# Performance work log

Hardware: AMD Instinct MI355X
Metric: run time of the kernel (lower is better)

The kernel has to match this reference:

```python
import jax, jax.numpy as jnp
import numpy as np


def _conv1x1(x, w, b=None):
    # x: (N,C,H,W), w: (O,C) -> (N,O,H,W)
    y = jnp.einsum('nchw,oc->nohw', x, w)
    return y if b is None else y + b[None, :, None, None]


def _norm(f):
    # per-channel zero-mean / unit-std over (N,H,W); torch.std is unbiased (ddof=1)
    mean = f.mean(axis=(0, 2, 3), keepdims=True)
    std = f.std(axis=(0, 2, 3), ddof=1, keepdims=True)
    return (f - mean) / (std + 1e-6)


def _causal_attention(x, w_cls):
    N, C, H, W = x.shape
    M = _conv1x1(x, w_cls).reshape(N, -1, H * W)     # (N,K,HW)
    sm = jax.nn.softmax(M, axis=2)                   # softmax over spatial
    return jnp.einsum('nkp,ncp->nkc', sm, x.reshape(N, C, H * W))  # (N,K,C)


def _ccnet(x, wq, bq, wk, bk, wv, bv, gamma1):
    B, C, H, W = x.shape
    q = _conv1x1(x, wq, bq)  # (B,Cq,H,W)
    k = _conv1x1(x, wk, bk)
    v = _conv1x1(x, wv, bv)  # (B,C,H,W)
    # column (vertical) attention energies with -inf on the self diagonal
    eH = jnp.einsum('bciw,bcjw->biwj', q, k)         # (B,H,W,H)
    eH = jnp.where(jnp.eye(H, dtype=bool)[None, :, None, :], -jnp.inf, eH)
    # row (horizontal) attention energies
    eW = jnp.einsum('bchi,bchj->bhij', q, k)         # (B,H,W,W)
    att = jax.nn.softmax(jnp.concatenate([eH, eW], axis=3), axis=3)
    attH, attW = att[..., :H], att[..., H:]
    outH = jnp.einsum('bcjw,biwj->bciw', v, attH)    # aggregate along column
    outW = jnp.einsum('bchj,bhij->bchi', v, attW)    # aggregate along row
    return gamma1 * (outH + outW) + x


def setup_inputs() -> dict:
    key = jax.random.key(0)
    ks = jax.random.split(key, 10)
    B, C, H, W = 8, 256, 96, 96
    Cq, K = C // 8, 6
    f32 = jnp.float32
    return {
        'preds_S': jax.random.normal(ks[0], (B, C, H, W), f32),
        'preds_T': jax.random.normal(ks[1], (B, C, H, W), f32),
        'w_cls': jax.random.normal(ks[2], (K, C), f32) * 0.05,
        'wq': jax.random.normal(ks[3], (Cq, C), f32) * 0.05,
        'bq': jnp.zeros((Cq,), f32),
        'wk': jax.random.normal(ks[4], (Cq, C), f32) * 0.05,
        'bk': jnp.zeros((Cq,), f32),
        'wv': jax.random.normal(ks[5], (C, C), f32) * 0.05,
        'bv': jnp.zeros((C,), f32),
        'gamma1': jax.random.normal(ks[6], (1,), f32) * 0.1,
    }


def reference(preds_S, preds_T, w_cls, wq, bq, wk, bk, wv, bv, gamma1):
    CA_W, CC_W = 0.0005, 1e-05
    N = preds_S.shape[0]
    s = _norm(preds_S)
    t = _norm(preds_T)
    ca_t = _causal_attention(t, w_cls)
    ca_s = _causal_attention(s, w_cls)
    ca_loss = jnp.sum((ca_t - ca_s) ** 2) / N
    cc_t = _ccnet(t, wq, bq, wk, bk, wv, bv, gamma1)
    cc_s = _ccnet(s, wq, bq, wk, bk, wv, bv, gamma1)
    cc_loss = jnp.sum((cc_t - cc_s) ** 2) / N
    return ca_loss * CA_W + cc_loss * CC_W
```

## Files before the change

### kernel.cpp

```cpp
#include <hip/hip_runtime.h>
#include <math.h>

#define NBAT 8
#define NC   256
#define NH   96
#define NW   96
#define NP   9216
#define NCQ  32
#define NKC  6
#define NV   320
#define NTOT 73728

typedef __attribute__((ext_vector_type(4))) float  floatx4;
typedef __attribute__((ext_vector_type(8))) short  short8;

__device__ __forceinline__ float bf2f(unsigned short h){
  return __uint_as_float(((unsigned)h) << 16);
}
__device__ __forceinline__ unsigned short f2bf(float f){
  unsigned u = __float_as_uint(f);
  u += 0x7FFFu + ((u >> 16) & 1u);
  return (unsigned short)(u >> 16);
}

union F4 { float4 v; float a[4]; };

__device__ __forceinline__ float warpReduceSum(float v){
  #pragma unroll
  for (int m = 32; m; m >>= 1) v += __shfl_xor(v, m);
  return v;
}
__device__ __forceinline__ float warpReduceMax(float v){
  #pragma unroll
  for (int m = 32; m; m >>= 1) v = fmaxf(v, __shfl_xor(v, m));
  return v;
}
__device__ float blockReduceSum(float v){
  __shared__ float lds[8];
  v = warpReduceSum(v);
  int wid = threadIdx.x >> 6, lane = threadIdx.x & 63;
  int nw = blockDim.x >> 6;
  if (lane == 0) lds[wid] = v;
  __syncthreads();
  if (wid == 0){
    v = (lane < nw) ? lds[lane] : 0.f;
    #pragma unroll
    for (int m = 4; m; m >>= 1) v += __shfl_xor(v, m);
  }
  __syncthreads();
  return v;
}
__device__ float blockReduceMax(float v){
  __shared__ float lds[8];
  v = warpReduceMax(v);
  int wid = threadIdx.x >> 6, lane = threadIdx.x & 63;
  int nw = blockDim.x >> 6;
  if (lane == 0) lds[wid] = v;
  __syncthreads();
  if (wid == 0){
    v = (lane < nw) ? lds[lane] : -INFINITY;
    #pragma unroll
    for (int m = 4; m; m >>= 1) v = fmaxf(v, __shfl_xor(v, m));
  }
  __syncthreads();
  return v;
}

__global__ __launch_bounds__(256)
void k_stats(const float* __restrict__ S, const float* __restrict__ T,
             float* __restrict__ s_sum, float* __restrict__ s_sq){
  int blk = blockIdx.x;
  int t = blk / (NC * NBAT);
  int rem = blk % (NC * NBAT);
  int c = rem / NBAT;
  int n = rem % NBAT;
  const float4* x4 = (const float4*)((t ? T : S) + ((size_t)n * NC + c) * NP);
  F4 f[9];
  #pragma unroll
  for (int j = 0; j < 9; j++) f[j].v = x4[threadIdx.x + j * 256];
  float s = 0.f, q = 0.f;
  #pragma unroll
  for (int j = 0; j < 9; j++)
    #pragma unroll
    for (int e = 0; e < 4; e++){ s += f[j].a[e]; q += f[j].a[e] * f[j].a[e]; }
  s = blockReduceSum(s);
  q = blockReduceSum(q);
  if (threadIdx.x == 0){
    atomicAdd(&s_sum[t * NC + c], s);
    atomicAdd(&s_sq[t * NC + c], q);
  }
}

__global__ __launch_bounds__(512)
void k_finalize(const float* __restrict__ s_sum, const float* __restrict__ s_sq,
                float* __restrict__ mean, float* __restrict__ inv){
  int i = threadIdx.x;
  if (i < 2 * NC){
    float s = s_sum[i], q = s_sq[i];
    float m = s / (float)NTOT;
    float var = (q - s * m) / (float)(NTOT - 1);
    var = fmaxf(var, 0.f);
    mean[i] = m;
    inv[i] = 1.f / (sqrtf(var) + 1e-6f);
  }
}

__global__ __launch_bounds__(256)
void k_xn(const float* __restrict__ S, const float* __restrict__ T, int b0,
          const float* __restrict__ mean, const float* __restrict__ inv,
          unsigned short* __restrict__ XNT, unsigned short* __restrict__ XNS){
  int pt = blockIdx.x, ct = blockIdx.y;
  int bb = blockIdx.z >> 1, ts = blockIdx.z & 1;
  int t = ts ? 0 : 1;
  const float* x0 = ts ? S : T;
  unsigned short* XN = (ts ? XNS : XNT) + (size_t)bb * NP * NC;
  int bg = b0 + bb;
  int p0 = pt * 64, c0 = ct * 64;
  __shared__ float tile[64 * 65];
  const float* x = x0 + ((size_t)bg * NC + c0) * NP + p0;
  #pragma unroll
  for (int i = 0; i < 4; i++){
    int idx = threadIdx.x + i * 256;
    int r = idx >> 4, g = (idx & 15) * 4;
    F4 f; f.v = *(const float4*)(x + (size_t)r * NP + g);
    float m = mean[t * NC + c0 + r], iv = inv[t * NC + c0 + r];
    #pragma unroll
    for (int j = 0; j < 4; j++) tile[(g + j) * 65 + r] = (f.a[j] - m) * iv;
  }
  __syncthreads();
  #pragma unroll
  for (int i = 0; i < 4; i++){
    int idx = threadIdx.x + i * 256;
    int p = idx >> 4, g = (idx & 15) * 4;
    unsigned lo = (unsigned)f2bf(tile[p * 65 + g + 0]) | ((unsigned)f2bf(tile[p * 65 + g + 1]) << 16);
    unsigned hi = (unsigned)f2bf(tile[p * 65 + g + 2]) | ((unsigned)f2bf(tile[p * 65 + g + 3]) << 16);
    uint2 u; u.x = lo; u.y = hi;
    *(uint2*)(XN + ((size_t)(p0 + p)) * NC + c0 + g) = u;
  }
}

__global__ __launch_bounds__(256)
void k_caM(const unsigned short* __restrict__ XNT, const unsigned short* __restrict__ XNS,
           const float* __restrict__ wcls, int b0,
           float* __restrict__ smca){
  int pt = blockIdx.x, bb = blockIdx.y, ts = blockIdx.z;
  int t = ts ? 0 : 1;
  const unsigned short* XN = (ts ? XNS : XNT) + (size_t)bb * NP * NC;
  __shared__ float wcf[NKC * NC];
  for (int idx = threadIdx.x; idx < NKC * NC; idx += 256) wcf[idx] = wcls[idx];
  __syncthreads();
  int p = pt * 256 + threadIdx.x;
  const unsigned short* row = XN + (size_t)p * NC;
  float acc[NKC];
  #pragma unroll
  for (int k = 0; k < NKC; k++) acc[k] = 0.f;
  for (int c = 0; c < NC; c += 8){
    short8 v = *(const short8*)(row + c);
    #pragma unroll
    for (int j = 0; j < 8; j++){
      float xv = bf2f((unsigned short)v[j]);
      #pragma unroll
      for (int k = 0; k < NKC; k++) acc[k] += wcf[k * NC + c + j] * xv;
    }
  }
  size_t base = ((size_t)(t * NBAT + b0 + bb) * NKC) * NP + p;
  #pragma unroll
  for (int k = 0; k < NKC; k++) smca[base + (size_t)k * NP] = acc[k];
}

__global__ __launch_bounds__(256)
void k_caSoftmax(float* __restrict__ smca, int b0){
  int r = blockIdx.x;
  int bb = r / (2 * NKC);
  int rem = r % (2 * NKC);
  int ts = rem / NKC, k = rem % NKC;
  int t = ts ? 0 : 1;
  float* row = smca + ((size_t)(t * NBAT + b0 + bb) * NKC + k) * NP;
  float m = -INFINITY;
  for (int p = threadIdx.x; p < NP; p += 256) m = fmaxf(m, row[p]);
  m = blockReduceMax(m);
  __shared__ float bm, bs;
  if (threadIdx.x == 0) bm = m;
  __syncthreads();
  m = bm;
  float s = 0.f;
  for (int p = threadIdx.x; p < NP; p += 256) s += expf(row[p] - m);
  s = blockReduceSum(s);
  if (threadIdx.x == 0) bs = 1.f / s;
  __syncthreads();
  float rs = bs;
  for (int p = threadIdx.x; p < NP; p += 256) row[p] = expf(row[p] - m) * rs;
}

__global__ __launch_bounds__(256)
void k_caOut(const unsigned short* __restrict__ XNT, const unsigned short* __restrict__ XNS,
             const float* __restrict__ smca, int b0,
             float* __restrict__ ca){
  int ks = blockIdx.x, bb = blockIdx.y, ts = blockIdx.z;
  int t = ts ? 0 : 1;
  const unsigned short* XN = (ts ? XNS : XNT) + (size_t)bb * NP * NC;
  int p0 = ks * 256;
  __shared__ float smt[NKC * 256];
  const float* smbase = smca + (size_t)(t * NBAT + b0 + bb) * NKC * NP;
  for (int idx = threadIdx.x; idx < NKC * 256; idx += 256){
    int k = idx >> 8, pp = idx & 255;
    smt[idx] = smbase[(size_t)k * NP + p0 + pp];
  }
  __syncthreads();
  int c = threadIdx.x;
  float acc[NKC];
  #pragma unroll
  for (int k = 0; k < NKC; k++) acc[k] = 0.f;
  const unsigned short* xp = XN + (size_t)p0 * NC + c;
  for (int pp = 0; pp < 256; pp++){
    float xv = bf2f(xp[(size_t)pp * NC]);
    #pragma unroll
    for (int k = 0; k < NKC; k++) acc[k] += smt[k * 256 + pp] * xv;
  }
  float* cab = ca + ((size_t)(t * NBAT + b0 + bb) * NKC) * NC + c;
  #pragma unroll
  for (int k = 0; k < NKC; k++) atomicAdd(&cab[(size_t)k * NC], acc[k]);
}

__global__ __launch_bounds__(256)
void k_caLoss(const float* __restrict__ ca, float* __restrict__ out){
  int i = blockIdx.x * 256 + threadIdx.x;
  float d = 0.f;
  if (i < NBAT * NKC * NC) d = ca[(size_t)NBAT * NKC * NC + i] - ca[i];
  float ss = blockReduceSum(d * d);
  if (threadIdx.x == 0) atomicAdd(out, ss * (0.0005f / 8.0f));
}

__global__ __launch_bounds__(256)
void k_wconv(const float* __restrict__ wv, const float* __restrict__ wq,
             const float* __restrict__ wk, unsigned short* __restrict__ Wb){
  int n = blockIdx.x;
  const float* src = (n < 256) ? (wv + (size_t)n * NC)
                   : (n < 288) ? (wq + (size_t)(n - 256) * NC)
                               : (wk + (size_t)(n - 288) * NC);
  Wb[(size_t)n * NC + threadIdx.x] = f2bf(src[threadIdx.x]);
}

__global__ __launch_bounds__(256)
void k_v(const unsigned short* __restrict__ XNT, const unsigned short* __restrict__ XNS,
         const unsigned short* __restrict__ Wb,
         const float* __restrict__ bv, const float* __restrict__ bq,
         const float* __restrict__ bk,
         unsigned short* __restrict__ V1T, unsigned short* __restrict__ V1S,
         unsigned short* __restrict__ qT, unsigned short* __restrict__ kT,
         unsigned short* __restrict__ qS, unsigned short* __restrict__ kS){
  int pt = blockIdx.x;
  int bb = blockIdx.y >> 1, ts = blockIdx.y & 1;
  const unsigned short* XN = (ts ? XNS : XNT) + (size_t)bb * NP * NC;
  unsigned short* V1 = (ts ? V1S : V1T) + (size_t)bb * NP * NC;
  unsigned short* qb  = (ts ? qS : qT) + (size_t)bb * NP * NCQ;
  unsigned short* kb  = (ts ? kS : kT) + (size_t)bb * NP * NCQ;
  int p0 = pt * 64;
  __shared__ unsigned short Wl[NV * 40];
  int lane = threadIdx.x & 63;
  int wid = threadIdx.x >> 6;
  int col = lane & 15, quad = lane >> 4;
  const unsigned short* xnb = XN + (size_t)(p0 + wid * 16 + col) * NC;
  floatx4 acc[20];
  #pragma unroll
  for (int nt = 0; nt < 20; nt++) acc[nt] = (floatx4){0.f, 0.f, 0.f, 0.f};

  int ci_n[5], ci_k8[5];
  #pragma unroll
  for (int i = 0; i < 5; i++){ int ci = i * 256 + threadIdx.x; ci_n[i] = ci >> 2; ci_k8[i] = (ci & 3) * 8; }

  short8 w[5];
  #pragma unroll
  for (int i = 0; i < 5; i++)
    w[i] = *(const short8*)(Wb + (size_t)ci_n[i] * NC + ci_k8[i]);

  for (int ks = 0; ks < 8; ks++){
    if (ks) __syncthreads();
    #pragma unroll
    for (int i = 0; i < 5; i++)
      *(short8*)(Wl + ci_n[i] * 40 + ci_k8[i]) = w[i];
    __syncthreads();
    if (ks < 7){
      int k0n = (ks + 1) * 32;
      #pragma unroll
      for (int i = 0; i < 5; i++)
        w[i] = *(const short8*)(Wb + (size_t)ci_n[i] * NC + k0n + ci_k8[i]);
    }
    short8 a = *(const short8*)(xnb + ks * 32 + quad * 8);
    #pragma unroll
    for (int nt = 0; nt < 20; nt++){
      short8 b = *(const short8*)(Wl + (nt * 16 + col) * 40 + quad * 8);
      acc[nt] = __builtin_amdgcn_mfma_f32_16x16x32_bf16(a, b, acc[nt], 0, 0, 0);
    }
  }

  int prow0 = p0 + wid * 16 + quad * 4;
  int hh = prow0 / 96, ww = prow0 % 96;
  #pragma unroll
  for (int nt = 0; nt < 16; nt++){
    int c = nt * 16 + col;
    float bias = bv[c];
    uint2 u;
    u.x = (unsigned)f2bf(acc[nt][0] + bias) | ((unsigned)f2bf(acc[nt][1] + bias) << 16);
    u.y = (unsigned)f2bf(acc[nt][2] + bias) | ((unsigned)f2bf(acc[nt][3] + bias) << 16);
    *(uint2*)(V1 + ((size_t)(hh * 256 + c)) * 96 + ww) = u;
  }
  #pragma unroll
  for (int nt = 16; nt < 18; nt++){
    int c = (nt - 16) * 16 + col;
    float bias = bq[c];
    #pragma unroll
    for (int i = 0; i < 4; i++)
      qb[((size_t)(prow0 + i)) * NCQ + c] = f2bf(acc[nt][i] + bias);
  }
  #pragma unroll
  for (int nt = 18; nt < 20; nt++){
    int c = (nt - 18) * 16 + col;
    float bias = bk[c];
    #pragma unroll
    for (int i = 0; i < 4; i++)
      kb[((size_t)(prow0 + i)) * NCQ + c] = f2bf(acc[nt][i] + bias);
  }
}

__global__ __launch_bounds__(256)
void k_vt(const unsigned short* __restrict__ V1T, const unsigned short* __restrict__ V1S,
          unsigned short* __restrict__ V2T, unsigned short* __restrict__ V2S){
  int cp = blockIdx.x;
  int bb = blockIdx.y >> 1, ts = blockIdx.y & 1;
  const unsigned short* V1 = (ts ? V1S : V1T) + (size_t)bb * NP * NC;
  unsigned short* V2 = (ts ? V2S : V2T) + (size_t)bb * NP * NC;
  int c0 = cp * 2;
  __shared__ unsigned short tile[2 * 96 * 104];
  #pragma unroll
  for (int k = 0; k < 9; k++){
    int idx = threadIdx.x + k * 256;
    int cl = idx / 1152, rem = idx % 1152;
    int h = rem / 12, g = rem % 12;
    short8 v = *(const short8*)(V1 + ((size_t)(h * 256 + c0 + cl)) * 96 + g * 8);
    #pragma unroll
    for (int jj = 0; jj < 8; jj++)
      tile[cl * 9984 + (g * 8 + jj) * 104 + h] = ((unsigned short*)&v)[jj];
  }
  __syncthreads();
  #pragma unroll
  for (int k = 0; k < 9; k++){
    int idx = threadIdx.x + k * 256;
    int cl = idx / 1152, rem = idx % 1152;
    int w = rem / 12, g = rem % 12;
    short8 v = *(const short8*)(tile + cl * 9984 + w * 104 + g * 8);
    *(short8*)(V2 + ((size_t)(w * 256 + c0 + cl)) * 96 + g * 8) = v;
  }
}

__global__ __launch_bounds__(256)
void k_e(const unsigned short* __restrict__ qT, const unsigned short* __restrict__ kT,
         const unsigned short* __restrict__ qS, const unsigned short* __restrict__ kS,
         unsigned short* __restrict__ attHtT, unsigned short* __restrict__ attWT,
         unsigned short* __restrict__ attHtS, unsigned short* __restrict__ attWS){
  int x = blockIdx.x, which = blockIdx.z;
  int bb = blockIdx.y >> 1, ts = blockIdx.y & 1;
  const unsigned short* qb = (ts ? qS : qT) + (size_t)bb * NP * NCQ;
  const unsigned short* kb = (ts ? kS : kT) + (size_t)bb * NP * NCQ;
  unsigned short* att = (which ? (ts ? attWS : attWT) : (ts ? attHtS : attHtT))
                        + (size_t)bb * NP * 96;
  int lane = threadIdx.x & 63, wid = threadIdx.x >> 6;
  int col = lane & 15, quad = lane >> 4;
  int mi0 = (wid & 1) * 3, ni0 = (wid >> 1) * 3;
  short8 a[3], b[3];
  if (which == 0){
    #pragma unroll
    for (int m = 0; m < 3; m++)
      a[m] = *(const short8*)(qb + ((size_t)(((mi0 + m) * 16 + col) * 96 + x)) * NCQ + quad * 8);
    #pragma unroll
    for (int n = 0; n < 3; n++)
      b[n] = *(const short8*)(kb + ((size_t)(((ni0 + n) * 16 + col) * 96 + x)) * NCQ + quad * 8);
  } else {
    #pragma unroll
    for (int m = 0; m < 3; m++)
      a[m] = *(const short8*)(qb + ((size_t)(x * 96 + (mi0 + m) * 16 + col)) * NCQ + quad * 8);
    #pragma unroll
    for (int n = 0; n < 3; n++)
      b[n] = *(const short8*)(kb + ((size_t)(x * 96 + (ni0 + n) * 16 + col)) * NCQ + quad * 8);
  }
  floatx4 acc[3][3];
  #pragma unroll
  for (int m = 0; m < 3; m++)
    #pragma unroll
    for (int n = 0; n < 3; n++){
      acc[m][n] = (floatx4){0.f, 0.f, 0.f, 0.f};
      acc[m][n] = __builtin_amdgcn_mfma_f32_16x16x32_bf16(a[m], b[n], acc[m][n], 0, 0, 0);
    }
  #pragma unroll
  for (int m = 0; m < 3; m++)
    #pragma unroll
    for (int n = 0; n < 3; n++){
      int j = (ni0 + n) * 16 + col;
      #pragma unroll
      for (int r = 0; r < 4; r++){
        int i = (mi0 + m) * 16 + quad * 4 + r;
        float v = (!which && j == i) ? -INFINITY : acc[m][n][r];
        att[((size_t)(x * 96 + i)) * 96 + j] = f2bf(v);
      }
    }
}

__global__ __launch_bounds__(256)
void k_attSoftmax(unsigned short* __restrict__ attHtT, unsigned short* __restrict__ attWT,
                  unsigned short* __restrict__ attHtS, unsigned short* __restrict__ attWS,
                  int nbp){
  int q = blockIdx.x * 4 + (threadIdx.x >> 6);
  int lane = threadIdx.x & 63;
  int sS = (q >= nbp);
  int ql = sS ? q - nbp : q;
  unsigned short* aHt = sS ? attHtS : attHtT;
  unsigned short* aW  = sS ? attWS  : attWT;
  int bb = ql / NP, p = ql % NP;
  unsigned short* rowW = aW  + ((size_t)(bb * NP + p)) * 96;
  unsigned short* rowH = aHt + ((size_t)(bb * NP + (p % 96) * 96 + p / 96)) * 96;
  float h0 = bf2f(rowH[lane]);
  float w0 = bf2f(rowW[lane]);
  float h1 = (lane < 32) ? bf2f(rowH[64 + lane]) : -INFINITY;
  float w1 = (lane < 32) ? bf2f(rowW[64 + lane]) : -INFINITY;
  float m = fmaxf(fmaxf(h0, h1), fmaxf(w0, w1));
  m = warpReduceMax(m);
  float xh0 = expf(h0 - m), xw0 = expf(w0 - m);
  float xh1 = (lane < 32) ? expf(h1 - m) : 0.f;
  float xw1 = (lane < 32) ? expf(w1 - m) : 0.f;
  float s = warpReduceSum(xh0 + xw0 + xh1 + xw1);
  float rs = 1.f / s;
  rowH[lane] = f2bf(xh0 * rs);
  rowW[lane] = f2bf(xw0 * rs);
  if (lane < 32){
    rowH[64 + lane] = f2bf(xh1 * rs);
    rowW[64 + lane] = f2bf(xw1 * rs);
  }
}

__global__ __launch_bounds__(256)
void k_outH(const unsigned short* __restrict__ V2T, const unsigned short* __restrict__ V2S,
            const unsigned short* __restrict__ attHtT, const unsigned short* __restrict__ attHtS,
            unsigned short* __restrict__ OHT, unsigned short* __restrict__ OHS){
  int w = blockIdx.x, cs = blockIdx.z;
  int bb = blockIdx.y >> 1, ts = blockIdx.y & 1;
  const unsigned short* V2 = (ts ? V2S : V2T) + (size_t)bb * NP * NC;
  const unsigned short* att = (ts ? attHtS : attHtT) + (size_t)bb * NP * 96;
  unsigned short* OH = (ts ? OHS : OHT) + (size_t)bb * NP * NC + (size_t)cs * NP * 64;
  int lane = threadIdx.x & 63, wid = threadIdx.x >> 6;
  int col = lane & 15, quad = lane >> 4;
  int cl = wid * 16 + col;
  int c = cs * 64 + cl;
  floatx4 acc[6];
  #pragma unroll
  for (int m = 0; m < 6; m++) acc[m] = (floatx4){0.f, 0.f, 0.f, 0.f};
  #pragma unroll
  for (int ks = 0; ks < 3; ks++){
    int k0 = ks * 32 + quad * 8;
    short8 a[6], b;
    #pragma unroll
    for (int m = 0; m < 6; m++)
      a[m] = *(const short8*)(att + ((size_t)(w * 96 + m * 16 + col)) * 96 + k0);
    b = *(const short8*)(V2 + ((size_t)(w * 256 + c)) * 96 + k0);
    #pragma unroll
    for (int m = 0; m < 6; m++)
      acc[m] = __builtin_amdgcn_mfma_f32_16x16x32_bf16(a[m], b, acc[m], 0, 0, 0);
  }
  #pragma unroll
  for (int m = 0; m < 6; m++){
    #pragma unroll
    for (int r = 0; r < 4; r++){
      int i = m * 16 + quad * 4 + r;
      OH[((size_t)(i * 96 + w)) * 64 + cl] = f2bf(acc[m][r]);
    }
  }
}

__global__ __launch_bounds__(256)
void k_outWL(const unsigned short* __restrict__ V1T, const unsigned short* __restrict__ attWT,
             const unsigned short* __restrict__ OHT,
             const unsigned short* __restrict__ V1S, const unsigned short* __restrict__ attWS,
             const unsigned short* __restrict__ OHS,
             const unsigned short* __restrict__ XNT, const unsigned short* __restrict__ XNS,
             const float* __restrict__ gamma,
             float* __restrict__ out){
  int h = blockIdx.x, bb = blockIdx.y, cs = blockIdx.z;
  size_t pb = (size_t)bb * NP * NC;
  int lane = threadIdx.x & 63, wid = threadIdx.x >> 6;
  int col = lane & 15, quad = lane >> 4;
  int cl = wid * 16 + col;
  int c  = cs * 64 + cl;

  __shared__ unsigned short ohTl[96 * 72];
  __shared__ unsigned short ohSl[96 * 72];
  __shared__ unsigned short dnl [96 * 72];

  const unsigned short* OHTb = OHT + pb + (size_t)cs * NP * 64 + (size_t)(h * 96) * 64;
  const unsigned short* OHSb = OHS + pb + (size_t)cs * NP * 64 + (size_t)(h * 96) * 64;
  #pragma unroll
  for (int k = 0; k < 3; k++){
    int g = threadIdx.x + k * 256;
    int i = g >> 3, cc = (g & 7) * 8;
    short8 ot = *(const short8*)(OHTb + g * 8);
    short8 os = *(const short8*)(OHSb + g * 8);
    size_t gx = pb + ((size_t)(h * 96 + i)) * NC + cs * 64 + cc;
    short8 xt = *(const short8*)(XNT + gx);
    short8 xs = *(const short8*)(XNS + gx);
    short8 dn;
    #pragma unroll
    for (int j = 0; j < 8; j++)
      ((unsigned short*)&dn)[j] = f2bf(bf2f((unsigned short)xt[j]) - bf2f((unsigned short)xs[j]));
    *(short8*)(ohTl + i * 72 + cc) = ot;
    *(short8*)(ohSl + i * 72 + cc) = os;
    *(short8*)(dnl  + i * 72 + cc) = dn;
  }
  __syncthreads();

  floatx4 accT[6], accS[6];
  #pragma unroll
  for (int m = 0; m < 6; m++){
    accT[m] = (floatx4){0.f, 0.f, 0.f, 0.f};
    accS[m] = (floatx4){0.f, 0.f, 0.f, 0.f};
  }
  #pragma unroll
  for (int ks = 0; ks < 3; ks++){
    int k0 = ks * 32 + quad * 8;
    short8 a[6], b;
    #pragma unroll
    for (int m = 0; m < 6; m++)
      a[m] = *(const short8*)(attWT + (size_t)bb * NP * 96 + ((size_t)(h * 96 + m * 16 + col)) * 96 + k0);
    b = *(const short8*)(V1T + pb + ((size_t)(h * 256 + c)) * 96 + k0);
    #pragma unroll
    for (int m = 0; m < 6; m++)
      accT[m] = __builtin_amdgcn_mfma_f32_16x16x32_bf16(a[m], b, accT[m], 0, 0, 0);
  }
  #pragma unroll
  for (int ks = 0; ks < 3; ks++){
    int k0 = ks * 32 + quad * 8;
    short8 a[6], b;
    #pragma unroll
    for (int m = 0; m < 6; m++)
      a[m] = *(const short8*)(attWS + (size_t)bb * NP * 96 + ((size_t)(h * 96 + m * 16 + col)) * 96 + k0);
    b = *(const short8*)(V1S + pb + ((size_t)(h * 256 + c)) * 96 + k0);
    #pragma unroll
    for (int m = 0; m < 6; m++)
      accS[m] = __builtin_amdgcn_mfma_f32_16x16x32_bf16(a[m], b, accS[m], 0, 0, 0);
  }

  float g = gamma[0];
  float ss = 0.f;
  #pragma unroll
  for (int m = 0; m < 6; m++){
    int i0 = m * 16 + quad * 4;
    #pragma unroll
    for (int r = 0; r < 4; r++){
      int i = i0 + r;
      float oT = accT[m][r] + bf2f(ohTl[i * 72 + cl]);
      float oS = accS[m][r] + bf2f(ohSl[i * 72 + cl]);
      float d = g * (oT - oS) + bf2f(dnl[i * 72 + cl]);
      ss += d * d;
    }
  }
  ss = blockReduceSum(ss);
  if (threadIdx.x == 0) atomicAdd(out, ss * (1e-5f / 8.0f));
}

extern "C" void kernel_launch(void* const* d_in, const int* in_sizes, int n_in,
                              void* d_out, int out_size, void* d_ws, size_t ws_size,
                              hipStream_t stream){
  (void)in_sizes; (void)n_in; (void)out_size;
  const float* S    = (const float*)d_in[0];
  const float* T    = (const float*)d_in[1];
  const float* wcls = (const float*)d_in[2];
  const float* wq   = (const float*)d_in[3];
  const float* bq   = (const float*)d_in[4];
  const float* wk   = (const float*)d_in[5];
  const float* bk   = (const float*)d_in[6];
  const float* wv   = (const float*)d_in[7];
  const float* bv   = (const float*)d_in[8];
  const float* gamma= (const float*)d_in[9];
  float* out = (float*)d_out;

  char* base = (char*)d_ws;
  size_t off = 0;
  auto alloc = [&](size_t b){ size_t o = off; off += (b + 255) & ~(size_t)255; return o; };
  size_t o_ssum = alloc(2 * NC * 4);
  size_t o_ssq  = alloc(2 * NC * 4);
  size_t o_mean = alloc(2 * NC * 4);
  size_t o_inv  = alloc(2 * NC * 4);
  size_t o_wb   = alloc((size_t)NV * NC * 2);
  size_t o_ca   = alloc((size_t)2 * NBAT * NKC * NC * 4);
  size_t o_smca = alloc((size_t)2 * NBAT * NKC * NP * 4);
  size_t fixed = off;

  const size_t PB  = (size_t)NP * NC * 2;
  const size_t AT1 = (size_t)NP * 96 * 2;
  const size_t QB  = (size_t)NP * NCQ * 2;
  size_t per_b = 8 * PB + 4 * AT1 + 4 * QB;
  int NB = 8;
  while (NB > 1 && fixed + (size_t)NB * per_b + 8192 > ws_size) NB >>= 1;

  size_t o_xnT = alloc((size_t)NB * PB);
  size_t o_xnS = alloc((size_t)NB * PB);
  size_t o_v1T = alloc((size_t)NB * PB);
  size_t o_v1S = alloc((size_t)NB * PB);
  size_t o_v2T = alloc((size_t)NB * PB);
  size_t o_v2S = alloc((size_t)NB * PB);
  size_t o_ohT = alloc((size_t)NB * PB);
  size_t o_ohS = alloc((size_t)NB * PB);
  size_t o_hT  = alloc((size_t)NB * AT1);
  size_t o_wT  = alloc((size_t)NB * AT1);
  size_t o_hS  = alloc((size_t)NB * AT1);
  size_t o_wS  = alloc((size_t)NB * AT1);
  size_t o_qT  = alloc((size_t)NB * QB);
  size_t o_kT  = alloc((size_t)NB * QB);
  size_t o_qS  = alloc((size_t)NB * QB);
  size_t o_kS  = alloc((size_t)NB * QB);

  float* ssum = (float*)(base + o_ssum);
  float* ssq  = (float*)(base + o_ssq);
  float* mean = (float*)(base + o_mean);
  float* inv  = (float*)(base + o_inv);
  float* ca   = (float*)(base + o_ca);
  float* smca = (float*)(base + o_smca);
  unsigned short* Wb   = (unsigned short*)(base + o_wb);
  unsigned short* XNT  = (unsigned short*)(base + o_xnT);
  unsigned short* XNS  = (unsigned short*)(base + o_xnS);
  unsigned short* V1T  = (unsigned short*)(base + o_v1T);
  unsigned short* V1S  = (unsigned short*)(base + o_v1S);
  unsigned short* V2T  = (unsigned short*)(base + o_v2T);
  unsigned short* V2S  = (unsigned short*)(base + o_v2S);
  unsigned short* OHT  = (unsigned short*)(base + o_ohT);
  unsigned short* OHS  = (unsigned short*)(base + o_ohS);
  unsigned short* aHtT = (unsigned short*)(base + o_hT);
  unsigned short* aWT  = (unsigned short*)(base + o_wT);
  unsigned short* aHtS = (unsigned short*)(base + o_hS);
  unsigned short* aWS  = (unsigned short*)(base + o_wS);
  unsigned short* qT   = (unsigned short*)(base + o_qT);
  unsigned short* kT   = (unsigned short*)(base + o_kT);
  unsigned short* qS   = (unsigned short*)(base + o_qS);
  unsigned short* kS   = (unsigned short*)(base + o_kS);

  hipMemsetAsync(d_out, 0, 4, stream);
  hipMemsetAsync(base + o_ssum, 0, 4096, stream);
  hipMemsetAsync(base + o_ca, 0, (size_t)2 * NBAT * NKC * NC * 4, stream);

  k_stats<<<dim3(2 * NC * NBAT), 256, 0, stream>>>(S, T, ssum, ssq);
  k_finalize<<<1, 512, 0, stream>>>(ssum, ssq, mean, inv);
  k_wconv<<<dim3(NV), 256, 0, stream>>>(wv, wq, wk, Wb);

  for (int b0 = 0; b0 < NBAT; b0 += NB){
    k_xn<<<dim3(144, 4, 2 * NB), 256, 0, stream>>>(S, T, b0, mean, inv, XNT, XNS);
    k_caM<<<dim3(36, NB, 2), 256, 0, stream>>>(XNT, XNS, wcls, b0, smca);
    k_caSoftmax<<<dim3(2 * NB * NKC), 256, 0, stream>>>(smca, b0);
    k_caOut<<<dim3(36, NB, 2), 256, 0, stream>>>(XNT, XNS, smca, b0, ca);
    k_v<<<dim3(144, 2 * NB), 256, 0, stream>>>(XNT, XNS, Wb, bv, bq, bk,
                                               V1T, V1S, qT, kT, qS, kS);
    k_vt<<<dim3(128, 2 * NB), 256, 0, stream>>>(V1T, V1S, V2T, V2S);
    k_e<<<dim3(96, 2 * NB, 2), 256, 0, stream>>>(qT, kT, qS, kS, aHtT, aWT, aHtS, aWS);
    k_attSoftmax<<<dim3(2 * NB * NP / 4), 256, 0, stream>>>(aHtT, aWT, aHtS, aWS, NB * NP);
    k_outH<<<dim3(96, 2 * NB, 4), 256, 0, stream>>>(V2T, V2S, aHtT, aHtS, OHT, OHS);
    k_outWL<<<dim3(96, NB, 4), 256, 0, stream>>>(V1T, aWT, OHT, V1S, aWS, OHS,
                                                 XNT, XNS, gamma, out);
  }
  k_caLoss<<<dim3(48), 256, 0, stream>>>(ca, out);
}
```

Before: 611.1 us.

## Fuse CA logits into normalize kernel, precompute T-S diff, alias V2 buffers

The normalization kernel now handles teacher and student in one block. It also writes a precomputed bf16 T−S difference and accumulates the class-attention logits through atomics. This removes the separate k_caM pass and the re-reading of both normalized tensors in k_outWL. V2 buffers are aliased onto the XN buffers to shrink the workspace, which may allow larger batch chunks. k_stats block indexing is reordered so consecutive blocks walk contiguous channels. The cost is an extra memset of smca, atomic adds across the four channel tiles, and one more full-size write of the difference tensor.

```diff
diff --git a/kernel.cpp b/kernel.cpp
--- a/kernel.cpp
+++ b/kernel.cpp
@@ -70,10 +70,9 @@
 void k_stats(const float* __restrict__ S, const float* __restrict__ T,
              float* __restrict__ s_sum, float* __restrict__ s_sq){
   int blk = blockIdx.x;
-  int t = blk / (NC * NBAT);
-  int rem = blk % (NC * NBAT);
-  int c = rem / NBAT;
-  int n = rem % NBAT;
+  int t = blk >> 11;
+  int n = (blk >> 8) & 7;
+  int c = blk & 255;
   const float4* x4 = (const float4*)((t ? T : S) + ((size_t)n * NC + c) * NP);
   F4 f[9];
   #pragma unroll
@@ -108,64 +107,85 @@
 __global__ __launch_bounds__(256)
 void k_xn(const float* __restrict__ S, const float* __restrict__ T, int b0,
           const float* __restrict__ mean, const float* __restrict__ inv,
-          unsigned short* __restrict__ XNT, unsigned short* __restrict__ XNS){
-  int pt = blockIdx.x, ct = blockIdx.y;
-  int bb = blockIdx.z >> 1, ts = blockIdx.z & 1;
-  int t = ts ? 0 : 1;
-  const float* x0 = ts ? S : T;
-  unsigned short* XN = (ts ? XNS : XNT) + (size_t)bb * NP * NC;
+          const float* __restrict__ wcls,
+          unsigned short* __restrict__ XNT, unsigned short* __restrict__ XNS,
+          unsigned short* __restrict__ DN,
+          float* __restrict__ smca){
+  int pt = blockIdx.x, ct = blockIdx.y, bb = blockIdx.z;
   int bg = b0 + bb;
   int p0 = pt * 64, c0 = ct * 64;
-  __shared__ float tile[64 * 65];
-  const float* x = x0 + ((size_t)bg * NC + c0) * NP + p0;
+  __shared__ float tT[64 * 65];
+  __shared__ float tS[64 * 65];
+  __shared__ float wl[NKC * 64];
+  for (int idx = threadIdx.x; idx < NKC * 64; idx += 256)
+    wl[idx] = wcls[(idx >> 6) * NC + c0 + (idx & 63)];
+  const float* xT = T + ((size_t)bg * NC + c0) * NP + p0;
+  const float* xS = S + ((size_t)bg * NC + c0) * NP + p0;
   #pragma unroll
   for (int i = 0; i < 4; i++){
     int idx = threadIdx.x + i * 256;
     int r = idx >> 4, g = (idx & 15) * 4;
-    F4 f; f.v = *(const float4*)(x + (size_t)r * NP + g);
-    float m = mean[t * NC + c0 + r], iv = inv[t * NC + c0 + r];
-    #pragma unroll
-    for (int j = 0; j < 4; j++) tile[(g + j) * 65 + r] = (f.a[j] - m) * iv;
-  }
-  __syncthreads();
+    F4 fT, fS;
+    fT.v = *(const float4*)(xT + (size_t)r * NP + g);
+    fS.v = *(const float4*)(xS + (size_t)r * NP + g);
+    float mT = mean[NC + c0 + r], ivT = inv[NC + c0 + r];
+    float mS = mean[c0 + r],      ivS = inv[c0 + r];
+    #pragma unroll
+    for (int j = 0; j < 4; j++){
+      tT[(g + j) * 65 + r] = (fT.a[j] - mT) * ivT;
+      tS[(g + j) * 65 + r] = (fS.a[j] - mS) * ivS;
+    }
+  }
+  __syncthreads();
+  size_t ob = (size_t)bb * NP * NC;
   #pragma unroll
   for (int i = 0; i < 4; i++){
     int idx = threadIdx.x + i * 256;
     int p = idx >> 4, g = (idx & 15) * 4;
-    unsigned lo = (unsigned)f2bf(tile[p * 65 + g + 0]) | ((unsigned)f2bf(tile[p * 65 + g + 1]) << 16);
-    unsigned hi = (unsigned)f2bf(tile[p * 65 + g + 2]) | ((unsigned)f2bf(tile[p * 65 + g + 3]) << 16);
-    uint2 u; u.x = lo; u.y = hi;
-    *(uint2*)(XN + ((size_t)(p0 + p)) * NC + c0 + g) = u;
-  }
-}
-
-__global__ __launch_bounds__(256)
-void k_caM(const unsigned short* __restrict__ XNT, const unsigned short* __restrict__ XNS,
-           const float* __restrict__ wcls, int b0,
-           float* __restrict__ smca){
-  int pt = blockIdx.x, bb = blockIdx.y, ts = blockIdx.z;
-  int t = ts ? 0 : 1;
-  const unsigned short* XN = (ts ? XNS : XNT) + (size_t)bb * NP * NC;
-  __shared__ float wcf[NKC * NC];
-  for (int idx = threadIdx.x; idx < NKC * NC; idx += 256) wcf[idx] = wcls[idx];
-  __syncthreads();
-  int p = pt * 256 + threadIdx.x;
-  const unsigned short* row = XN + (size_t)p * NC;
-  float acc[NKC];
-  #pragma unroll
-  for (int k = 0; k < NKC; k++) acc[k] = 0.f;
-  for (int c = 0; c < NC; c += 8){
-    short8 v = *(const short8*)(row + c);
-    #pragma unroll
-    for (int j = 0; j < 8; j++){
-      float xv = bf2f((unsigned short)v[j]);
-      #pragma unroll
-      for (int k = 0; k < NKC; k++) acc[k] += wcf[k * NC + c + j] * xv;
-    }
-  }
-  size_t base = ((size_t)(t * NBAT + b0 + bb) * NKC) * NP + p;
-  #pragma unroll
-  for (int k = 0; k < NKC; k++) smca[base + (size_t)k * NP] = acc[k];
+    float vT0 = tT[p * 65 + g + 0], vT1 = tT[p * 65 + g + 1];
+    float vT2 = tT[p * 65 + g + 2], vT3 = tT[p * 65 + g + 3];
+    float vS0 = tS[p * 65 + g + 0], vS1 = tS[p * 65 + g + 1];
+    float vS2 = tS[p * 65 + g + 2], vS3 = tS[p * 65 + g + 3];
+    size_t oa = ob + ((size_t)(p0 + p)) * NC + c0 + g;
+    uint2 u;
+    u.x = (unsigned)f2bf(vT0) | ((unsigned)f2bf(vT1) << 16);
+    u.y = (unsigned)f2bf(vT2) | ((unsigned)f2bf(vT3) << 16);
+    *(uint2*)(XNT + oa) = u;
+    u.x = (unsigned)f2bf(vS0) | ((unsigned)f2bf(vS1) << 16);
+    u.y = (unsigned)f2bf(vS2) | ((unsigned)f2bf(vS3) << 16);
+    *(uint2*)(XNS + oa) = u;
+    u.x = (unsigned)f2bf(vT0 - vS0) | ((unsigned)f2bf(vT1 - vS1) << 16);
+    u.y = (unsigned)f2bf(vT2 - vS2) | ((unsigned)f2bf(vT3 - vS3) << 16);
+    *(uint2*)(DN + oa) = u;
+  }
+  int p = threadIdx.x >> 2, sub = threadIdx.x & 3;
+  float aT[NKC], aS[NKC];
+  #pragma unroll
+  for (int k = 0; k < NKC; k++){ aT[k] = 0.f; aS[k] = 0.f; }
+  #pragma unroll
+  for (int c16 = 0; c16 < 16; c16++){
+    int cc = sub * 16 + c16;
+    float xvT = tT[p * 65 + cc], xvS = tS[p * 65 + cc];
+    #pragma unroll
+    for (int k = 0; k < NKC; k++){
+      aT[k] += wl[k * 64 + cc] * xvT;
+      aS[k] += wl[k * 64 + cc] * xvS;
+    }
+  }
+  #pragma unroll
+  for (int k = 0; k < NKC; k++){
+    aT[k] += __shfl_xor(aT[k], 1); aT[k] += __shfl_xor(aT[k], 2);
+    aS[k] += __shfl_xor(aS[k], 1); aS[k] += __shfl_xor(aS[k], 2);
+  }
+  if (sub == 0){
+    float* mTp = smca + ((size_t)(NBAT + bg) * NKC) * NP + (p0 + p);
+    float* mSp = smca + ((size_t)bg * NKC) * NP + (p0 + p);
+    #pragma unroll
+    for (int k = 0; k < NKC; k++){
+      atomicAdd(&mTp[(size_t)k * NP], aT[k]);
+      atomicAdd(&mSp[(size_t)k * NP], aS[k]);
+    }
+  }
 }
 
 __global__ __launch_bounds__(256)
@@ -480,7 +500,7 @@
              const unsigned short* __restrict__ OHT,
              const unsigned short* __restrict__ V1S, const unsigned short* __restrict__ attWS,
              const unsigned short* __restrict__ OHS,
-             const unsigned short* __restrict__ XNT, const unsigned short* __restrict__ XNS,
+             const unsigned short* __restrict__ DN,
              const float* __restrict__ gamma,
              float* __restrict__ out){
   int h = blockIdx.x, bb = blockIdx.y, cs = blockIdx.z;
@@ -496,19 +516,14 @@
 
   const unsigned short* OHTb = OHT + pb + (size_t)cs * NP * 64 + (size_t)(h * 96) * 64;
   const unsigned short* OHSb = OHS + pb + (size_t)cs * NP * 64 + (size_t)(h * 96) * 64;
+  const unsigned short* DNb  = DN + pb;
   #pragma unroll
   for (int k = 0; k < 3; k++){
     int g = threadIdx.x + k * 256;
     int i = g >> 3, cc = (g & 7) * 8;
     short8 ot = *(const short8*)(OHTb + g * 8);
     short8 os = *(const short8*)(OHSb + g * 8);
-    size_t gx = pb + ((size_t)(h * 96 + i)) * NC + cs * 64 + cc;
-    short8 xt = *(const short8*)(XNT + gx);
-    short8 xs = *(const short8*)(XNS + gx);
-    short8 dn;
-    #pragma unroll
-    for (int j = 0; j < 8; j++)
-      ((unsigned short*)&dn)[j] = f2bf(bf2f((unsigned short)xt[j]) - bf2f((unsigned short)xs[j]));
+    short8 dn = *(const short8*)(DNb + ((size_t)(h * 96 + i)) * NC + cs * 64 + cc);
     *(short8*)(ohTl + i * 72 + cc) = ot;
     *(short8*)(ohSl + i * 72 + cc) = os;
     *(short8*)(dnl  + i * 72 + cc) = dn;
@@ -595,16 +610,15 @@
   const size_t PB  = (size_t)NP * NC * 2;
   const size_t AT1 = (size_t)NP * 96 * 2;
   const size_t QB  = (size_t)NP * NCQ * 2;
-  size_t per_b = 8 * PB + 4 * AT1 + 4 * QB;
+  size_t per_b = 7 * PB + 4 * AT1 + 4 * QB;
   int NB = 8;
   while (NB > 1 && fixed + (size_t)NB * per_b + 8192 > ws_size) NB >>= 1;
 
   size_t o_xnT = alloc((size_t)NB * PB);
   size_t o_xnS = alloc((size_t)NB * PB);
+  size_t o_dn  = alloc((size_t)NB * PB);
   size_t o_v1T = alloc((size_t)NB * PB);
   size_t o_v1S = alloc((size_t)NB * PB);
-  size_t o_v2T = alloc((size_t)NB * PB);
-  size_t o_v2S = alloc((size_t)NB * PB);
   size_t o_ohT = alloc((size_t)NB * PB);
   size_t o_ohS = alloc((size_t)NB * PB);
   size_t o_hT  = alloc((size_t)NB * AT1);
@@ -625,10 +639,11 @@
   unsigned short* Wb   = (unsigned short*)(base + o_wb);
   unsigned short* XNT  = (unsigned short*)(base + o_xnT);
   unsigned short* XNS  = (unsigned short*)(base + o_xnS);
+  unsigned short* DN   = (unsigned short*)(base + o_dn);
   unsigned short* V1T  = (unsigned short*)(base + o_v1T);
   unsigned short* V1S  = (unsigned short*)(base + o_v1S);
-  unsigned short* V2T  = (unsigned short*)(base + o_v2T);
-  unsigned short* V2S  = (unsigned short*)(base + o_v2S);
+  unsigned short* V2T  = XNT;
+  unsigned short* V2S  = XNS;
   unsigned short* OHT  = (unsigned short*)(base + o_ohT);
   unsigned short* OHS  = (unsigned short*)(base + o_ohS);
   unsigned short* aHtT = (unsigned short*)(base + o_hT);
@@ -643,14 +658,15 @@
   hipMemsetAsync(d_out, 0, 4, stream);
   hipMemsetAsync(base + o_ssum, 0, 4096, stream);
   hipMemsetAsync(base + o_ca, 0, (size_t)2 * NBAT * NKC * NC * 4, stream);
+  hipMemsetAsync(base + o_smca, 0, (size_t)2 * NBAT * NKC * NP * 4, stream);
 
   k_stats<<<dim3(2 * NC * NBAT), 256, 0, stream>>>(S, T, ssum, ssq);
   k_finalize<<<1, 512, 0, stream>>>(ssum, ssq, mean, inv);
   k_wconv<<<dim3(NV), 256, 0, stream>>>(wv, wq, wk, Wb);
 
   for (int b0 = 0; b0 < NBAT; b0 += NB){
-    k_xn<<<dim3(144, 4, 2 * NB), 256, 0, stream>>>(S, T, b0, mean, inv, XNT, XNS);
-    k_caM<<<dim3(36, NB, 2), 256, 0, stream>>>(XNT, XNS, wcls, b0, smca);
+    k_xn<<<dim3(144, 4, NB), 256, 0, stream>>>(S, T, b0, mean, inv, wcls,
+                                               XNT, XNS, DN, smca);
     k_caSoftmax<<<dim3(2 * NB * NKC), 256, 0, stream>>>(smca, b0);
     k_caOut<<<dim3(36, NB, 2), 256, 0, stream>>>(XNT, XNS, smca, b0, ca);
     k_v<<<dim3(144, 2 * NB), 256, 0, stream>>>(XNT, XNS, Wb, bv, bq, bk,
@@ -660,7 +676,7 @@
     k_attSoftmax<<<dim3(2 * NB * NP / 4), 256, 0, stream>>>(aHtT, aWT, aHtS, aWS, NB * NP);
     k_outH<<<dim3(96, 2 * NB, 4), 256, 0, stream>>>(V2T, V2S, aHtT, aHtS, OHT, OHS);
     k_outWL<<<dim3(96, NB, 4), 256, 0, stream>>>(V1T, aWT, OHT, V1S, aWS, OHS,
-                                                 XNT, XNS, gamma, out);
+                                                 DN, gamma, out);
   }
   k_caLoss<<<dim3(48), 256, 0, stream>>>(ca, out);
 }
```

Measured after the change: 593.6 us. -2.9%, faster.
